# Performance work log

Measured on AMD Instinct MI355X. Metric: run time of the kernel, lower is better.

Reference implementation:

```python
import jax, jax.numpy as jnp
import numpy as np

N = 100000      # nodes
E = 1600000     # directed edges
F_IN = 128      # input features
H = 64          # hidden_channels
C = 32          # num_classes


def setup_inputs() -> dict:
    key = jax.random.key(0)
    ks = jax.random.split(key, 8)
    x = jax.random.normal(ks[0], (N, F_IN), jnp.float32)
    edge_index = jax.random.randint(ks[1], (2, E), 0, N, jnp.int32)
    W1 = jax.random.normal(ks[2], (F_IN, H), jnp.float32) * (1.0 / np.sqrt(F_IN))
    b1 = jnp.zeros((H,), jnp.float32)
    W2 = jax.random.normal(ks[3], (H, H), jnp.float32) * (1.0 / np.sqrt(H))
    b2 = jnp.zeros((H,), jnp.float32)
    Wout = jax.random.normal(ks[4], (H, C), jnp.float32) * (1.0 / np.sqrt(H))
    bout = jnp.zeros((C,), jnp.float32)
    return {"x": x, "edge_index": edge_index, "W1": W1, "b1": b1,
            "W2": W2, "b2": b2, "Wout": Wout, "bout": bout}


def gcn_conv(x, W, b, src, dst, n):
    """PyG GCNConv: out = D^-1/2 (A + I) D^-1/2 (X W) + b,
    with degree computed on A + I."""
    h = x @ W  # [N, out]
    ones = jnp.ones(dst.shape[0], h.dtype)
    deg = jax.ops.segment_sum(ones, dst, num_segments=n) + 1.0  # self-loop
    dinv = jax.lax.rsqrt(deg)                                   # [N]
    coef = dinv[src] * dinv[dst]                                # [E]
    agg = jax.ops.segment_sum(h[src] * coef[:, None], dst, num_segments=n)
    agg = agg + h * (dinv * dinv)[:, None]                      # self-loop message
    return agg + b


def reference(x, edge_index, W1, b1, W2, b2, Wout, bout):
    src, dst = edge_index[0], edge_index[1]
    n = x.shape[0]
    h = jax.nn.relu(gcn_conv(x, W1, b1, src, dst, n))
    # dropout(p=0.5) is a no-op in eval mode
    h = jax.nn.relu(gcn_conv(h, W2, b2, src, dst, n))
    return jax.nn.softmax(h @ Wout + bout, axis=1)
```

## Files before the change

kernel.cpp:

```cpp
#include <hip/hip_runtime.h>
#include <stdint.h>


typedef unsigned short u16;
typedef unsigned int u32;
typedef __attribute__((ext_vector_type(8))) short bf16x8;
typedef __attribute__((ext_vector_type(4))) float f32x4;

#define GN 100000
#define GE 1600000
#define NBKT 196
#define BCAP 10240
#define EBLK 782

__device__ __forceinline__ float bf2f(u32 lo16) {
  union { u32 i; float f; } v; v.i = lo16 << 16; return v.f;
}
__device__ __forceinline__ u16 f2bf(float f) {
  union { float f; u32 i; } v; v.f = f;
  u32 x = v.i;
  u32 r = x + 0x7fffu + ((x >> 16) & 1u);
  return (u16)(r >> 16);
}
__device__ __forceinline__ u32 pack2(float a, float b) {
  return (u32)f2bf(a) | ((u32)f2bf(b) << 16);
}

__global__ __launch_bounds__(256) void k_detect(const u16* __restrict__ xs,
                                                int* __restrict__ flag,
                                                int* __restrict__ ccount) {
  __shared__ int cnt;
  if (threadIdx.x == 0) cnt = 0;
  if (threadIdx.x < NBKT) ccount[threadIdx.x] = 0;
  __syncthreads();
  int w = 0;
#pragma unroll
  for (int i = 0; i < 16; i++) {
    int s = threadIdx.x * 16 + i;
    u32 u = xs[(size_t)s * 1562];
    u32 ex = (u >> 7) & 0xffu;
    if (ex == 0xffu || ex < 0x40u) w++;
  }
  atomicAdd(&cnt, w);
  __syncthreads();
  if (threadIdx.x == 0) flag[0] = (cnt >= 64) ? 0 : 1;
}

__global__ __launch_bounds__(256) void k_partA(const int* __restrict__ src,
                                               const int* __restrict__ dst,
                                               int* __restrict__ ccount, int E,
                                               const void* p2, const void* p3,
                                               const void* p4, const void* p5,
                                               const void* p6, const void* p7,
                                               const int* __restrict__ flag,
                                               float* __restrict__ Wf,
                                               u16* __restrict__ Wb1,
                                               u16* __restrict__ Wb2,
                                               u16* __restrict__ Wbo,
                                               u32* __restrict__ pairs) {
  int tid = threadIdx.x;
  if (blockIdx.x >= EBLK) {
    int i = (blockIdx.x - EBLK) * 256 + tid;
    bool isbf = flag[0] != 0;
    if (i < 14496) {
      const void* sp; int off;
      if (i < 8192)       { sp = p2; off = i; }
      else if (i < 8256)  { sp = p3; off = i - 8192; }
      else if (i < 12352) { sp = p4; off = i - 8256; }
      else if (i < 12416) { sp = p5; off = i - 12352; }
      else if (i < 14464) { sp = p6; off = i - 12416; }
      else                { sp = p7; off = i - 14464; }
      Wf[i] = isbf ? bf2f((u32)((const u16*)sp)[off]) : ((const float*)sp)[off];
    } else if (i < 14496 + 12288) {
      int idx = i - 14496;
      const void* W; u16* dstp;
      if (idx < 8192) { W = p2; dstp = Wb1; }
      else            { W = p4; dstp = Wb2; idx -= 8192; }
      int j  = idx & 7;
      int l  = (idx >> 3) & 63;
      int c  = (idx >> 9) & 3;
      int kc = idx >> 11;
      int k = kc * 32 + (l >> 4) * 8 + j;
      int n = c * 16 + (l & 15);
      dstp[idx] = isbf ? ((const u16*)W)[k * 64 + n]
                       : f2bf(((const float*)W)[k * 64 + n]);
    } else if (i < 14496 + 12288 + 2048) {
      int idx = i - 14496 - 12288;
      int j  = idx & 7;
      int l  = (idx >> 3) & 63;
      int c  = (idx >> 9) & 1;
      int kc = idx >> 10;
      int k = kc * 32 + (l >> 4) * 8 + j;
      int n = c * 16 + (l & 15);
      Wbo[idx] = isbf ? ((const u16*)p6)[k * 32 + n]
                      : f2bf(((const float*)p6)[k * 32 + n]);
    }
    return;
  }
  __shared__ int hist[256];
  __shared__ int off[256];
  hist[tid] = 0;
  __syncthreads();
  int e0 = (blockIdx.x * 256 + tid) * 8;
  int s_[8], d_[8];
  int cnt = 0;
  if (e0 + 8 <= E) {
    const int4* sp = (const int4*)(src + e0);
    const int4* dp = (const int4*)(dst + e0);
#pragma unroll
    for (int q = 0; q < 2; q++) {
      int4 sv = sp[q], dv = dp[q];
      s_[4 * q + 0] = sv.x; s_[4 * q + 1] = sv.y;
      s_[4 * q + 2] = sv.z; s_[4 * q + 3] = sv.w;
      d_[4 * q + 0] = dv.x; d_[4 * q + 1] = dv.y;
      d_[4 * q + 2] = dv.z; d_[4 * q + 3] = dv.w;
    }
    cnt = 8;
  } else {
    for (int q = 0; q < 8 && e0 + q < E; q++) {
      s_[q] = src[e0 + q]; d_[q] = dst[e0 + q]; cnt++;
    }
  }
  for (int q = 0; q < cnt; q++) atomicAdd(&hist[d_[q] >> 9], 1);
  __syncthreads();
  if (tid < NBKT && hist[tid] > 0)
    off[tid] = tid * BCAP + atomicAdd(&ccount[tid], hist[tid]);
  __syncthreads();
  for (int q = 0; q < cnt; q++) {
    int bkt = d_[q] >> 9;
    int pos = atomicAdd(&off[bkt], 1);
    pairs[pos] = ((u32)s_[q] << 9) | ((u32)d_[q] & 511u);
  }
}

__global__ __launch_bounds__(256) void k_partB(const u32* __restrict__ pairs,
                                               const int* __restrict__ ccount,
                                               int* __restrict__ rpx,
                                               float* __restrict__ dinv,
                                               int* __restrict__ ssort, int N) {
  __shared__ int cnt[512];
  __shared__ int sc[256];
  int b = blockIdx.x;
  int tid = threadIdx.x;
  int nb0 = b << 9;
  int beg = b * BCAP, end = beg + ccount[b];
  cnt[tid] = 0; cnt[tid + 256] = 0;
  __syncthreads();
  for (int i = beg + tid; i < end; i += 256) {
    u32 p = pairs[i];
    atomicAdd(&cnt[p & 511u], 1);
  }
  __syncthreads();
  int c0 = cnt[2 * tid], c1 = cnt[2 * tid + 1];
  int s = c0 + c1;
  sc[tid] = s;
  __syncthreads();
#pragma unroll
  for (int off = 1; off < 256; off <<= 1) {
    int a = (tid >= off) ? sc[tid - off] : 0;
    __syncthreads();
    sc[tid] += a;
    __syncthreads();
  }
  int excl = sc[tid] - s;
  cnt[2 * tid] = excl;
  cnt[2 * tid + 1] = excl + c0;
  int idx = b * 513 + 2 * tid;
  rpx[idx]     = beg + excl;
  rpx[idx + 1] = beg + excl + c0;
  if (tid == 255) rpx[b * 513 + 512] = end;
  int n0 = nb0 + 2 * tid, n1 = n0 + 1;
  if (n0 < N) dinv[n0] = rsqrtf((float)c0 + 1.0f);
  if (n1 < N) dinv[n1] = rsqrtf((float)c1 + 1.0f);
  __syncthreads();
  for (int i = beg + tid; i < end; i += 256) {
    u32 p = pairs[i];
    int pos = beg + atomicAdd(&cnt[p & 511u], 1);
    ssort[pos] = (int)(p >> 9);
  }
}

template <int K, int XMODE>
__global__ __launch_bounds__(256) void k_mgemm(const void* __restrict__ X,
                                               const u16* __restrict__ Wb,
                                               const float* __restrict__ dinv,
                                               const int* __restrict__ flag,
                                               u16* __restrict__ out, int M) {
  constexpr int NKC = K / 32;
  constexpr int P = K + 8;
  __shared__ u16 Bs[NKC * 4 * 64 * 8];
  __shared__ u16 As[128 * P];
  int tid = threadIdx.x;
  bool isbf = (XMODE == 1) ? true : (flag[0] != 0);
#pragma unroll
  for (int i = 0; i < NKC; i++)
    ((uint4*)Bs)[i * 256 + tid] = ((const uint4*)Wb)[i * 256 + tid];

  int rowbase = blockIdx.x * 128;
  int rowsValid = M - rowbase; if (rowsValid > 128) rowsValid = 128;
  if (isbf) {
    constexpr int F8 = K / 8;
    constexpr int NL = K / 16;
    const uint4* Xg = (const uint4*)X;
    uint4 v[NL];
#pragma unroll
    for (int i = 0; i < NL; i++) {
      int q = i * 256 + tid;
      int row = q / F8, c8 = q % F8;
      v[i] = (row < rowsValid) ? Xg[(size_t)(rowbase + row) * F8 + c8]
                               : make_uint4(0, 0, 0, 0);
    }
#pragma unroll
    for (int i = 0; i < NL; i++) {
      int q = i * 256 + tid;
      int row = q / F8, c8 = q % F8;
      *(uint4*)&As[row * P + c8 * 8] = v[i];
    }
  } else {
    constexpr int F4 = K / 4;
    constexpr int NL = K / 8;
    const float4* Xg = (const float4*)X;
    float4 v[NL];
#pragma unroll
    for (int i = 0; i < NL; i++) {
      int q = i * 256 + tid;
      int row = q / F4, c4 = q % F4;
      v[i] = (row < rowsValid) ? Xg[(size_t)(rowbase + row) * F4 + c4]
                               : make_float4(0.f, 0.f, 0.f, 0.f);
    }
#pragma unroll
    for (int i = 0; i < NL; i++) {
      int q = i * 256 + tid;
      int row = q / F4, c4 = q % F4;
      u32* d = (u32*)&As[row * P + c4 * 4];
      d[0] = pack2(v[i].x, v[i].y);
      d[1] = pack2(v[i].z, v[i].w);
    }
  }
  __syncthreads();

  int lane = tid & 63, wave = tid >> 6;
  int m0 = lane & 15;
  int koff = (lane >> 4) * 8;
  f32x4 acc[2][4];
#pragma unroll
  for (int t = 0; t < 2; t++)
#pragma unroll
    for (int c = 0; c < 4; c++) acc[t][c] = (f32x4){0.f, 0.f, 0.f, 0.f};

#pragma unroll
  for (int kc = 0; kc < NKC; kc++) {
    union { uint4 v; bf16x8 s; } a[2];
#pragma unroll
    for (int t = 0; t < 2; t++) {
      int rl = wave * 32 + t * 16 + m0;
      a[t].v = *(const uint4*)&As[rl * P + kc * 32 + koff];
    }
#pragma unroll
    for (int c = 0; c < 4; c++) {
      bf16x8 b = *(const bf16x8*)&Bs[((kc * 4 + c) * 64 + lane) * 8];
      acc[0][c] = __builtin_amdgcn_mfma_f32_16x16x32_bf16(a[0].s, b, acc[0][c], 0, 0, 0);
      acc[1][c] = __builtin_amdgcn_mfma_f32_16x16x32_bf16(a[1].s, b, acc[1][c], 0, 0, 0);
    }
  }
  __syncthreads();
  int cl = lane & 15, rq = (lane >> 4) * 4;
#pragma unroll
  for (int t = 0; t < 2; t++)
#pragma unroll
    for (int reg = 0; reg < 4; reg++) {
      int rl = wave * 32 + t * 16 + rq + reg;
      int r = rowbase + rl;
      float s = (r < M) ? dinv[r] : 0.f;
#pragma unroll
      for (int c = 0; c < 4; c++)
        As[rl * P + c * 16 + cl] = f2bf(acc[t][c][reg] * s);
    }
  __syncthreads();
  uint4* outg = (uint4*)out;
#pragma unroll
  for (int i = 0; i < 4; i++) {
    int q = i * 256 + tid;
    int row = q >> 3, c8 = q & 7;
    int r = rowbase + row;
    if (r < M) outg[(size_t)r * 8 + c8] = *(uint4*)&As[row * P + c8 * 8];
  }
}

template <int MODE>
__global__ __launch_bounds__(256) void k_pullg(const u16* __restrict__ g,
                                               const int* __restrict__ rpx,
                                               const int* __restrict__ ss,
                                               const float* __restrict__ dinv,
                                               const float* __restrict__ bias,
                                               const u16* __restrict__ Wfrag,
                                               const float* __restrict__ bof,
                                               const int* __restrict__ flag,
                                               void* __restrict__ outv) {
  constexpr int P = 72;
  __shared__ u16 Hs[32 * P];
  __shared__ u16 Cs[(MODE == 0) ? 32 * P : 1];
  int tid = threadIdx.x;
  int lane = tid & 63, wave = tid >> 6;

  constexpr int NCF = (MODE == 0) ? 4 : 2;
  int c0 = (MODE == 0) ? ((wave >> 1) << 1) : 0;
  bf16x8 bfr[2][2];
#pragma unroll
  for (int kc = 0; kc < 2; kc++)
#pragma unroll
    for (int cc = 0; cc < 2; cc++)
      bfr[kc][cc] = *(const bf16x8*)&Wfrag[((kc * NCF + c0 + cc) * 64 + lane) * 8];

  int oct = tid >> 3;
  int node = blockIdx.x * 32 + oct;
  int fq = tid & 7;
  const uint4* gp4 = (const uint4*)g;
  int rix = node + (node >> 9);
  int beg = rpx[rix], end = rpx[rix + 1];

  uint4 sv = gp4[(size_t)node * 8 + fq];
  float acc[8];
  acc[0] = bf2f(sv.x & 0xffffu); acc[1] = bf2f(sv.x >> 16);
  acc[2] = bf2f(sv.y & 0xffffu); acc[3] = bf2f(sv.y >> 16);
  acc[4] = bf2f(sv.z & 0xffffu); acc[5] = bf2f(sv.z >> 16);
  acc[6] = bf2f(sv.w & 0xffffu); acc[7] = bf2f(sv.w >> 16);

#define ACC8(v)                                                      \
  do {                                                               \
    acc[0] += bf2f((v).x & 0xffffu); acc[1] += bf2f((v).x >> 16);    \
    acc[2] += bf2f((v).y & 0xffffu); acc[3] += bf2f((v).y >> 16);    \
    acc[4] += bf2f((v).z & 0xffffu); acc[5] += bf2f((v).z >> 16);    \
    acc[6] += bf2f((v).w & 0xffffu); acc[7] += bf2f((v).w >> 16);    \
  } while (0)

  int e = beg;
  for (; e + 4 <= end; e += 4) {
    int i0 = ss[e], i1 = ss[e + 1], i2 = ss[e + 2], i3 = ss[e + 3];
    uint4 v0 = gp4[(size_t)i0 * 8 + fq];
    uint4 v1 = gp4[(size_t)i1 * 8 + fq];
    uint4 v2 = gp4[(size_t)i2 * 8 + fq];
    uint4 v3 = gp4[(size_t)i3 * 8 + fq];
    ACC8(v0); ACC8(v1); ACC8(v2); ACC8(v3);
  }
  for (; e < end; e++) {
    int i0 = ss[e];
    uint4 v0 = gp4[(size_t)i0 * 8 + fq];
    ACC8(v0);
  }
#undef ACC8

  float dv = dinv[node];
  float4 b0 = ((const float4*)bias)[fq * 2];
  float4 b1 = ((const float4*)bias)[fq * 2 + 1];
  float r0 = fmaxf(dv * acc[0] + b0.x, 0.f);
  float r1 = fmaxf(dv * acc[1] + b0.y, 0.f);
  float r2 = fmaxf(dv * acc[2] + b0.z, 0.f);
  float r3 = fmaxf(dv * acc[3] + b0.w, 0.f);
  float r4 = fmaxf(dv * acc[4] + b1.x, 0.f);
  float r5 = fmaxf(dv * acc[5] + b1.y, 0.f);
  float r6 = fmaxf(dv * acc[6] + b1.z, 0.f);
  float r7 = fmaxf(dv * acc[7] + b1.w, 0.f);
  *(uint4*)&Hs[oct * P + fq * 8] =
      make_uint4(pack2(r0, r1), pack2(r2, r3), pack2(r4, r5), pack2(r6, r7));
  __syncthreads();

  int m0 = lane & 15;
  int koff = (lane >> 4) * 8;
  int rt = wave & 1;
  f32x4 cacc[2];
  cacc[0] = (f32x4){0.f, 0.f, 0.f, 0.f};
  cacc[1] = (f32x4){0.f, 0.f, 0.f, 0.f};
  if (MODE == 0 || wave < 2) {
#pragma unroll
    for (int kc = 0; kc < 2; kc++) {
      union { uint4 v; bf16x8 s; } a;
      a.v = *(const uint4*)&Hs[(rt * 16 + m0) * P + kc * 32 + koff];
      cacc[0] = __builtin_amdgcn_mfma_f32_16x16x32_bf16(a.s, bfr[kc][0], cacc[0], 0, 0, 0);
      cacc[1] = __builtin_amdgcn_mfma_f32_16x16x32_bf16(a.s, bfr[kc][1], cacc[1], 0, 0, 0);
    }
  }
  int cl = lane & 15, rq = (lane >> 4) * 4;
  if (MODE == 0) {
#pragma unroll
    for (int reg = 0; reg < 4; reg++) {
      int rl = rt * 16 + rq + reg;
      float s = dinv[blockIdx.x * 32 + rl];
      Cs[rl * P + (c0 + 0) * 16 + cl] = f2bf(cacc[0][reg] * s);
      Cs[rl * P + (c0 + 1) * 16 + cl] = f2bf(cacc[1][reg] * s);
    }
    __syncthreads();
    uint4* og = (uint4*)outv;
    int row = tid >> 3, c8 = tid & 7;
    og[(size_t)(blockIdx.x * 32 + row) * 8 + c8] = *(uint4*)&Cs[row * P + c8 * 8];
  } else if (wave < 2) {
    bool isbf = flag[0] != 0;
    float bb0 = bof[cl], bb1 = bof[16 + cl];
#pragma unroll
    for (int reg = 0; reg < 4; reg++) {
      int r = blockIdx.x * 32 + rt * 16 + rq + reg;
      float v0 = cacc[0][reg] + bb0;
      float v1 = cacc[1][reg] + bb1;
      float mx = fmaxf(v0, v1);
      mx = fmaxf(mx, __shfl_xor(mx, 1));
      mx = fmaxf(mx, __shfl_xor(mx, 2));
      mx = fmaxf(mx, __shfl_xor(mx, 4));
      mx = fmaxf(mx, __shfl_xor(mx, 8));
      float e0 = __expf(v0 - mx), e1 = __expf(v1 - mx);
      float s = e0 + e1;
      s += __shfl_xor(s, 1);
      s += __shfl_xor(s, 2);
      s += __shfl_xor(s, 4);
      s += __shfl_xor(s, 8);
      float inv = 1.f / s;
      if (isbf) {
        u16* go = (u16*)outv;
        go[(size_t)r * 32 + cl]      = f2bf(e0 * inv);
        go[(size_t)r * 32 + 16 + cl] = f2bf(e1 * inv);
      } else {
        float* go = (float*)outv;
        go[(size_t)r * 32 + cl]      = e0 * inv;
        go[(size_t)r * 32 + 16 + cl] = e1 * inv;
      }
    }
  }
}

extern "C" void kernel_launch(void* const* d_in, const int* in_sizes, int n_in,
                              void* d_out, int out_size, void* d_ws, size_t ws_size,
                              hipStream_t stream) {
  (void)in_sizes; (void)n_in; (void)out_size; (void)ws_size;
  const void* x  = d_in[0];
  const int* ei  = (const int*)d_in[1];
  const int E = GE;
  const int* srcI = ei;
  const int* dstI = ei + E;

  char* ws = (char*)d_ws;
  int*   flag   = (int*)(ws + 0);
  int*   ccount = (int*)(ws + 256);
  int*   rpx    = (int*)(ws + 4096);
  float* dinv   = (float*)(ws + 406528);
  float* Wf     = (float*)(ws + 806656);
  u16*   Wb1    = (u16*)(ws + 864768);
  u16*   Wb2    = (u16*)(ws + 881280);
  u16*   Wbo    = (u16*)(ws + 889600);
  int*   ssort  = (int*)(ws + 893952);
  u32*   pairs  = (u32*)(ws + 8922112);
  u16*   gA     = (u16*)(ws + 8922112);
  u16*   gB     = (u16*)(ws + 21722368);

  float* b1f = Wf + 8192;
  float* b2f = Wf + 12352;
  float* bof = Wf + 14464;

  k_detect<<<1, 256, 0, stream>>>((const u16*)x, flag, ccount);
  k_partA<<<EBLK + 113, 256, 0, stream>>>(srcI, dstI, ccount, E,
                                          d_in[2], d_in[3], d_in[4], d_in[5],
                                          d_in[6], d_in[7], flag,
                                          Wf, Wb1, Wb2, Wbo, pairs);
  k_partB<<<NBKT, 256, 0, stream>>>(pairs, ccount, rpx, dinv, ssort, GN);

  k_mgemm<128, 0><<<782, 256, 0, stream>>>(x, Wb1, dinv, flag, gA, GN);
  k_pullg<0><<<3125, 256, 0, stream>>>(gA, rpx, ssort, dinv, b1f, Wb2, bof, flag, gB);
  k_pullg<1><<<3125, 256, 0, stream>>>(gB, rpx, ssort, dinv, b2f, Wbo, bof, flag, d_out);
}
```

Measured before the change: 235.9 us.

## Stage bucketed edge scatter in LDS and use packed float2 gather accumulation

The bucketing kernel now builds a block-local prefix scan of bucket counts and stages the packed edge pairs in shared memory, then writes them out contiguously per bucket. This replaces scattered per-edge global writes with more coalesced ones. In the aggregation kernel, bf16 unpacking now feeds float2 vector adds so packed FP32 adds can be used, and the neighbor gather loop is unrolled to 8 loads in flight. The cost is extra LDS usage and scan barriers in the bucketing kernel, plus higher register pressure from the deeper unroll.

```diff
diff --git a/kernel.cpp b/kernel.cpp
--- a/kernel.cpp
+++ b/kernel.cpp
@@ -6,6 +6,7 @@
 typedef unsigned int u32;
 typedef __attribute__((ext_vector_type(8))) short bf16x8;
 typedef __attribute__((ext_vector_type(4))) float f32x4;
+typedef __attribute__((ext_vector_type(2))) float f32x2;
 
 #define GN 100000
 #define GE 1600000
@@ -24,6 +25,11 @@
 }
 __device__ __forceinline__ u32 pack2(float a, float b) {
   return (u32)f2bf(a) | ((u32)f2bf(b) << 16);
+}
+__device__ __forceinline__ f32x2 unpk(u32 u) {
+  union { u32 i; float f; } lo, hi;
+  lo.i = u << 16; hi.i = u & 0xffff0000u;
+  return (f32x2){lo.f, hi.f};
 }
 
 __global__ __launch_bounds__(256) void k_detect(const u16* __restrict__ xs,
@@ -98,7 +104,13 @@
     return;
   }
   __shared__ int hist[256];
-  __shared__ int off[256];
+  __shared__ int boff[256];
+  __shared__ int fill[256];
+  __shared__ int gbase[256];
+  __shared__ int sc[256];
+  __shared__ u32 buf[2048];
+  __shared__ int adr[2048];
+  __shared__ int stotal;
   hist[tid] = 0;
   __syncthreads();
   int e0 = (blockIdx.x * 256 + tid) * 8;
@@ -123,14 +135,31 @@
   }
   for (int q = 0; q < cnt; q++) atomicAdd(&hist[d_[q] >> 9], 1);
   __syncthreads();
-  if (tid < NBKT && hist[tid] > 0)
-    off[tid] = tid * BCAP + atomicAdd(&ccount[tid], hist[tid]);
+  int v = hist[tid];
+  sc[tid] = v;
+  __syncthreads();
+#pragma unroll
+  for (int off = 1; off < 256; off <<= 1) {
+    int a = (tid >= off) ? sc[tid - off] : 0;
+    __syncthreads();
+    sc[tid] += a;
+    __syncthreads();
+  }
+  int excl = sc[tid] - v;
+  boff[tid] = excl;
+  fill[tid] = excl;
+  if (tid == 255) stotal = sc[255];
+  if (tid < NBKT && v > 0) gbase[tid] = tid * BCAP + atomicAdd(&ccount[tid], v);
   __syncthreads();
   for (int q = 0; q < cnt; q++) {
     int bkt = d_[q] >> 9;
-    int pos = atomicAdd(&off[bkt], 1);
-    pairs[pos] = ((u32)s_[q] << 9) | ((u32)d_[q] & 511u);
-  }
+    int p = atomicAdd(&fill[bkt], 1);
+    buf[p] = ((u32)s_[q] << 9) | ((u32)d_[q] & 511u);
+    adr[p] = gbase[bkt] + (p - boff[bkt]);
+  }
+  __syncthreads();
+  int total = stotal;
+  for (int j = tid; j < total; j += 256) pairs[adr[j]] = buf[j];
 }
 
 __global__ __launch_bounds__(256) void k_partB(const u32* __restrict__ pairs,
@@ -320,28 +349,39 @@
   int beg = rpx[rix], end = rpx[rix + 1];
 
   uint4 sv = gp4[(size_t)node * 8 + fq];
-  float acc[8];
-  acc[0] = bf2f(sv.x & 0xffffu); acc[1] = bf2f(sv.x >> 16);
-  acc[2] = bf2f(sv.y & 0xffffu); acc[3] = bf2f(sv.y >> 16);
-  acc[4] = bf2f(sv.z & 0xffffu); acc[5] = bf2f(sv.z >> 16);
-  acc[6] = bf2f(sv.w & 0xffffu); acc[7] = bf2f(sv.w >> 16);
-
-#define ACC8(v)                                                      \
-  do {                                                               \
-    acc[0] += bf2f((v).x & 0xffffu); acc[1] += bf2f((v).x >> 16);    \
-    acc[2] += bf2f((v).y & 0xffffu); acc[3] += bf2f((v).y >> 16);    \
-    acc[4] += bf2f((v).z & 0xffffu); acc[5] += bf2f((v).z >> 16);    \
-    acc[6] += bf2f((v).w & 0xffffu); acc[7] += bf2f((v).w >> 16);    \
+  f32x2 acc2[4];
+  acc2[0] = unpk(sv.x); acc2[1] = unpk(sv.y);
+  acc2[2] = unpk(sv.z); acc2[3] = unpk(sv.w);
+
+#define ACC8(v)                                             \
+  do {                                                      \
+    acc2[0] += unpk((v).x); acc2[1] += unpk((v).y);         \
+    acc2[2] += unpk((v).z); acc2[3] += unpk((v).w);         \
   } while (0)
 
   int e = beg;
-  for (; e + 4 <= end; e += 4) {
+  for (; e + 8 <= end; e += 8) {
+    int i0 = ss[e],     i1 = ss[e + 1], i2 = ss[e + 2], i3 = ss[e + 3];
+    int i4 = ss[e + 4], i5 = ss[e + 5], i6 = ss[e + 6], i7 = ss[e + 7];
+    uint4 v0 = gp4[(size_t)i0 * 8 + fq];
+    uint4 v1 = gp4[(size_t)i1 * 8 + fq];
+    uint4 v2 = gp4[(size_t)i2 * 8 + fq];
+    uint4 v3 = gp4[(size_t)i3 * 8 + fq];
+    uint4 v4 = gp4[(size_t)i4 * 8 + fq];
+    uint4 v5 = gp4[(size_t)i5 * 8 + fq];
+    uint4 v6 = gp4[(size_t)i6 * 8 + fq];
+    uint4 v7 = gp4[(size_t)i7 * 8 + fq];
+    ACC8(v0); ACC8(v1); ACC8(v2); ACC8(v3);
+    ACC8(v4); ACC8(v5); ACC8(v6); ACC8(v7);
+  }
+  if (e + 4 <= end) {
     int i0 = ss[e], i1 = ss[e + 1], i2 = ss[e + 2], i3 = ss[e + 3];
     uint4 v0 = gp4[(size_t)i0 * 8 + fq];
     uint4 v1 = gp4[(size_t)i1 * 8 + fq];
     uint4 v2 = gp4[(size_t)i2 * 8 + fq];
     uint4 v3 = gp4[(size_t)i3 * 8 + fq];
     ACC8(v0); ACC8(v1); ACC8(v2); ACC8(v3);
+    e += 4;
   }
   for (; e < end; e++) {
     int i0 = ss[e];
@@ -353,14 +393,14 @@
   float dv = dinv[node];
   float4 b0 = ((const float4*)bias)[fq * 2];
   float4 b1 = ((const float4*)bias)[fq * 2 + 1];
-  float r0 = fmaxf(dv * acc[0] + b0.x, 0.f);
-  float r1 = fmaxf(dv * acc[1] + b0.y, 0.f);
-  float r2 = fmaxf(dv * acc[2] + b0.z, 0.f);
-  float r3 = fmaxf(dv * acc[3] + b0.w, 0.f);
-  float r4 = fmaxf(dv * acc[4] + b1.x, 0.f);
-  float r5 = fmaxf(dv * acc[5] + b1.y, 0.f);
-  float r6 = fmaxf(dv * acc[6] + b1.z, 0.f);
-  float r7 = fmaxf(dv * acc[7] + b1.w, 0.f);
+  float r0 = fmaxf(dv * acc2[0].x + b0.x, 0.f);
+  float r1 = fmaxf(dv * acc2[0].y + b0.y, 0.f);
+  float r2 = fmaxf(dv * acc2[1].x + b0.z, 0.f);
+  float r3 = fmaxf(dv * acc2[1].y + b0.w, 0.f);
+  float r4 = fmaxf(dv * acc2[2].x + b1.x, 0.f);
+  float r5 = fmaxf(dv * acc2[2].y + b1.y, 0.f);
+  float r6 = fmaxf(dv * acc2[3].x + b1.z, 0.f);
+  float r7 = fmaxf(dv * acc2[3].y + b1.w, 0.f);
   *(uint4*)&Hs[oct * P + fq * 8] =
       make_uint4(pack2(r0, r1), pack2(r2, r3), pack2(r4, r5), pack2(r6, r7));
   __syncthreads();
```

Result: no change. 236.2 us (+0.1%).
